# Kernel tuning notes

Hardware: AMD Instinct MI355X
Metric: run time of the kernel (lower is better)

The kernel has to match this reference:

```python
import jax, jax.numpy as jnp
import numpy as np

SENS = 200
DM = 128
NMAPS = 2
NLAYERS = 2
TH = 0.01
EPS = 1e-5
BATCH = 8
SEQ = 96
HEADS = 8


def setup_inputs() -> dict:
    key = jax.random.key(0)
    ks = jax.random.split(key, 8)
    x = jax.random.normal(ks[0], (BATCH, SENS, SEQ, DM), jnp.float32)
    attn_s = jax.random.uniform(ks[1], (1, BATCH, HEADS, SENS, SENS), jnp.float32)
    supports = jax.random.uniform(ks[2], (SENS, SENS), jnp.float32)
    W_conv = jax.random.normal(ks[3], (NMAPS, NLAYERS, DM, DM), jnp.float32) * 0.05
    b_conv = jnp.zeros((NMAPS, NLAYERS, DM), jnp.float32)
    bn_gamma = jnp.ones((NMAPS, DM), jnp.float32)
    bn_beta = jnp.zeros((NMAPS, DM), jnp.float32)
    W_out = jax.random.normal(ks[4], (NMAPS * DM, DM), jnp.float32) * 0.05
    b_out = jnp.zeros((DM,), jnp.float32)
    return dict(x=x, attn_s=attn_s, supports=supports, W_conv=W_conv,
                b_conv=b_conv, bn_gamma=bn_gamma, bn_beta=bn_beta,
                W_out=W_out, b_out=b_out)


def _process_map(A):
    # make_symmetric: lower triangle + mirrored strict lower triangle
    A = jnp.tril(A) + jnp.tril(A, -1).T
    # clamp: threshold on absolute value; note original returns |A| thresholded
    Aa = jnp.abs(A)
    A = jnp.where(Aa > TH, Aa, jnp.zeros_like(Aa))
    # SparseTensor.from_dense(A).t()
    return A.T


def _gcn_norm(adj_t):
    # GCNConv default: add self-loops (weight 1), symmetric D^-1/2 A D^-1/2
    A = adj_t + jnp.eye(adj_t.shape[0], dtype=adj_t.dtype)
    deg = A.sum(axis=1)
    d = jnp.where(deg > 0, jax.lax.rsqrt(deg), jnp.zeros_like(deg))
    return d[:, None] * A * d[None, :]


def reference(x, attn_s, supports, W_conv, b_conv, bn_gamma, bn_beta, W_out, b_out):
    B, N, S, D = x.shape
    # reshape_mat: [B,N,S,D] -> [B*S, N, D]
    xr = x.transpose(0, 2, 1, 3).reshape(B * S, N, D)

    # supports: [data map, adaptive map from attention (mean over batch, heads)]
    maps = [_process_map(supports), _process_map(attn_s[0].mean(axis=(0, 1)))]

    gcn_outputs = []
    for i in range(NMAPS):
        An = _gcn_norm(maps[i])  # [N,N]
        h = jnp.zeros_like(xr[..., :1]) * 0.0  # placeholder replaced below
        h = None
        for l in range(NLAYERS):
            xw = jnp.einsum('bnf,fg->bng', xr, W_conv[i, l])
            hl = jnp.einsum('mn,bng->bmg', An, xw) + b_conv[i, l]
            h = hl if h is None else h + hl
        # BatchNorm1d over feature channel (training-mode batch stats, biased var)
        mu = h.mean(axis=(0, 1))
        var = h.var(axis=(0, 1))
        hn = (h - mu) * jax.lax.rsqrt(var + EPS) * bn_gamma[i] + bn_beta[i]
        gcn_outputs.append(jax.nn.relu(hn))

    cat = jnp.concatenate(gcn_outputs, axis=-1)  # [B*S, N, NMAPS*DM]
    y = jax.nn.relu(jnp.einsum('bnc,cd->bnd', cat, W_out) + b_out)
    # inverse_reshape_mat: [B*S, N, D] -> [B, N, S, D]
    return y.reshape(B, S, N, D).transpose(0, 2, 1, 3)
```

## Files before the change

kernel.cpp:

```cpp
#include <hip/hip_runtime.h>

#define SENS 200
#define DM 128
#define SEQ 96
#define NB 8
#define BS 768
#define NTOT 153600
#define TH 0.01f
#define BN_EPS 1e-5f
#define MPAD 224
#define KP 208
#define XWROW 212
#define ASROW 76

typedef __attribute__((ext_vector_type(8)))  __bf16 bf16x8;
typedef __attribute__((ext_vector_type(4)))  __bf16 bf16x4;
typedef __attribute__((ext_vector_type(16))) float  f32x16;

__device__ __forceinline__ f32x16 mfma32(bf16x8 a, bf16x8 b, f32x16 c) {
    return __builtin_amdgcn_mfma_f32_32x32x16_bf16(a, b, c, 0, 0, 0);
}
__device__ __forceinline__ bf16x8 join8(bf16x4 a, bf16x4 b) {
    bf16x8 r;
    #pragma unroll
    for (int j = 0; j < 4; ++j) { r[j] = a[j]; r[j + 4] = b[j]; }
    return r;
}

__global__ void attn_mean_kernel(const float* __restrict__ attn, float* __restrict__ mapA) {
    int idx = blockIdx.x * 256 + threadIdx.x;
    if (idx >= SENS * SENS) return;
    float s = 0.f;
    #pragma unroll 8
    for (int q = 0; q < 64; ++q) s += attn[(size_t)q * SENS * SENS + idx];
    mapA[idx] = s * (1.0f / 64.0f);
}

__global__ void build_map_kernel(const float* __restrict__ supports, const float* __restrict__ mapA,
                                 float* __restrict__ M, float* __restrict__ deg) {
    __shared__ float red[256];
    int m = blockIdx.x, map = blockIdx.y, j = threadIdx.x;
    const float* src = (map == 0) ? supports : mapA;
    float v = 0.f;
    if (j < SENS) {
        float sym = (m >= j) ? src[m * SENS + j] : src[j * SENS + m];
        float a = fabsf(sym);
        v = (a > TH) ? a : 0.f;
        M[(size_t)map * SENS * SENS + m * SENS + j] = v;
    }
    red[j] = v;
    __syncthreads();
    for (int off = 128; off > 0; off >>= 1) {
        if (j < off) red[j] += red[j + off];
        __syncthreads();
    }
    if (j == 0) deg[map * SENS + m] = red[0] + 1.0f;
}

__global__ __launch_bounds__(256) void prep2_kernel(
    const float* __restrict__ x, const float* __restrict__ M, const float* __restrict__ deg,
    const float* __restrict__ W_conv, const float* __restrict__ b_conv,
    const float* __restrict__ W_out,
    __bf16* __restrict__ xk, __bf16* __restrict__ Anb,
    __bf16* __restrict__ Wt, __bf16* __restrict__ Wot,
    float* __restrict__ bsum, float* __restrict__ bnacc)
{
    const int bid = blockIdx.x, t = threadIdx.x;
    if (bid < BS) {
        const int bs = bid, b = bs / SEQ, s = bs % SEQ;
        const int fq = t & 31, sub = t >> 5;
        const float* xp = x + ((size_t)b * SENS) * SEQ * DM + (size_t)s * DM + fq * 4;
        __bf16* xo = xk + ((size_t)bs * 8 + (fq >> 2)) * MPAD * 16 + (fq & 3) * 4;
        for (int n = sub; n < MPAD; n += 8) {
            float4 v = make_float4(0.f, 0.f, 0.f, 0.f);
            if (n < SENS) v = *(const float4*)(xp + (size_t)n * SEQ * DM);
            bf16x4 o;
            o[0] = (__bf16)v.x; o[1] = (__bf16)v.y; o[2] = (__bf16)v.z; o[3] = (__bf16)v.w;
            *(bf16x4*)(xo + (size_t)n * 16) = o;
        }
    } else if (bid < BS + 2 * MPAD) {
        const int i = bid - BS, map = i / MPAD, m = i % MPAD;
        const int j = t;
        if (j < KP) {
            float val = 0.f;
            if (m < SENS && j < SENS) {
                float a = M[((size_t)map * SENS + m) * SENS + j] + ((m == j) ? 1.f : 0.f);
                val = rsqrtf(deg[map * SENS + m]) * a * rsqrtf(deg[map * SENS + j]);
            }
            Anb[(((size_t)map * 13 + (j >> 4)) * MPAD + m) * 16 + (j & 15)] = (__bf16)val;
        }
    } else {
        const int idx = (bid - (BS + 2 * MPAD)) * 256 + t;
        if (idx < 32768) {
            const int map = idx >> 14, g = (idx >> 7) & 127, f = idx & 127;
            const float* wp = W_conv + (size_t)map * 2 * DM * DM + f * DM + g;
            Wt[(((size_t)map * 8 + (f >> 4)) * DM + g) * 16 + (f & 15)] = (__bf16)(wp[0] + wp[DM * DM]);
        } else if (idx < 65536) {
            const int k = idx - 32768, d = k >> 8, c = k & 255;
            Wot[(((size_t)(c >> 4)) * DM + d) * 16 + (c & 15)] = (__bf16)W_out[c * DM + d];
        } else if (idx < 65792) {
            const int k = idx - 65536, map = k >> 7, g = k & 127;
            bsum[k] = b_conv[(map * 2) * DM + g] + b_conv[(map * 2 + 1) * DM + g];
        } else if (idx < 66304) {
            bnacc[idx - 65792] = 0.f;
        }
    }
}

__global__ __launch_bounds__(448) void conv_kernel(
    const __bf16* __restrict__ xk, const __bf16* __restrict__ Anb,
    const __bf16* __restrict__ Wt, const float* __restrict__ bsum,
    __bf16* __restrict__ h, float* __restrict__ bnacc)
{
    __shared__ __bf16 xw[128 * XWROW];
    const int bs = blockIdx.x, map = blockIdx.y;
    const int t = threadIdx.x, w = t >> 6, lane = t & 63;
    const int l31 = lane & 31, hi = lane >> 5;

    const __bf16* xb = xk + (((size_t)bs * 8) * MPAD + w * 32 + l31) * 16 + hi * 8;
    #pragma unroll
    for (int gh = 0; gh < 2; ++gh) {
        f32x16 acc[2];
        #pragma unroll
        for (int p = 0; p < 2; ++p)
            #pragma unroll
            for (int r = 0; r < 16; ++r) acc[p][r] = 0.f;
        const __bf16* wb = Wt + (((size_t)map * 8) * DM + gh * 64 + l31) * 16 + hi * 8;
        #pragma unroll
        for (int kc = 0; kc < 8; ++kc) {
            bf16x8 bfrag = *(const bf16x8*)(xb + (size_t)kc * MPAD * 16);
            #pragma unroll
            for (int p = 0; p < 2; ++p)
                acc[p] = mfma32(*(const bf16x8*)(wb + ((size_t)kc * DM + p * 32) * 16), bfrag, acc[p]);
        }
        if (w < 6 || l31 < 16) {
            #pragma unroll
            for (int p = 0; p < 2; ++p)
                #pragma unroll
                for (int r = 0; r < 16; ++r) {
                    const int row = gh * 64 + p * 32 + (r & 3) + 8 * (r >> 2) + 4 * hi;
                    xw[row * XWROW + w * 32 + l31] = (__bf16)acc[p][r];
                }
        }
    }
    __syncthreads();

    float bsn[4], bsq[4];
    const __bf16* ab = Anb + (((size_t)map * 13) * MPAD + w * 32 + l31) * 16 + hi * 8;
    #pragma unroll
    for (int cth = 0; cth < 2; ++cth) {
        f32x16 acc2[2];
        #pragma unroll
        for (int p = 0; p < 2; ++p)
            #pragma unroll
            for (int r = 0; r < 16; ++r) acc2[p][r] = 0.f;
        #pragma unroll
        for (int kc = 0; kc < 13; ++kc) {
            bf16x8 afrag = *(const bf16x8*)(ab + (size_t)kc * MPAD * 16);
            #pragma unroll
            for (int p = 0; p < 2; ++p) {
                const __bf16* pp = &xw[((cth * 2 + p) * 32 + l31) * XWROW + kc * 16 + hi * 8];
                acc2[p] = mfma32(afrag, join8(*(const bf16x4*)pp, *(const bf16x4*)(pp + 4)), acc2[p]);
            }
        }
        #pragma unroll
        for (int p = 0; p < 2; ++p) {
            const int ct = cth * 2 + p;
            const float bias = bsum[map * DM + ct * 32 + l31];
            bf16x8 h0, h1;
            float s = 0.f, q = 0.f;
            #pragma unroll
            for (int r = 0; r < 16; ++r) {
                const float v = acc2[p][r] + bias;
                if (r < 8) h0[r] = (__bf16)v; else h1[r - 8] = (__bf16)v;
                const int m = w * 32 + (r & 3) + 8 * (r >> 2) + 4 * hi;
                if (m < SENS) { s += v; q += v * v; }
            }
            __bf16* hp = h + ((((size_t)(bs * 2 + map) * 7 + w) * 4 + ct) * 64 + lane) * 16;
            *(bf16x8*)hp = h0;
            *(bf16x8*)(hp + 8) = h1;
            s += __shfl_xor(s, 32);
            q += __shfl_xor(q, 32);
            bsn[ct] = s; bsq[ct] = q;
        }
    }
    __syncthreads();
    float* red = (float*)xw;
    if (hi == 0) {
        #pragma unroll
        for (int ct = 0; ct < 4; ++ct) {
            red[(ct * 32 + l31) * 7 + w] = bsn[ct];
            red[(128 + ct * 32 + l31) * 7 + w] = bsq[ct];
        }
    }
    __syncthreads();
    if (t < 256) {
        const int sq = t >> 7, g = t & 127;
        float s = 0.f;
        #pragma unroll
        for (int k = 0; k < 7; ++k) s += red[(sq * 128 + g) * 7 + k];
        atomicAdd(&bnacc[sq * 256 + map * DM + g], s);
    }
}

__global__ __launch_bounds__(512) void out_kernel(
    const __bf16* __restrict__ h, const __bf16* __restrict__ Wot,
    const float* __restrict__ bnacc,
    const float* __restrict__ gamma, const float* __restrict__ beta,
    const float* __restrict__ b_out, float* __restrict__ out)
{
    __shared__ __bf16 As[MPAD * ASROW];
    __shared__ float sc_s[256], sh_s[256];
    const int bs = blockIdx.x;
    const int b = bs / SEQ, s = bs % SEQ;
    const int t = threadIdx.x, w = t >> 6, lane = t & 63;
    const int l31 = lane & 31, hi = lane >> 5;
    const int dct = w & 3, sbase = w >> 2;
    if (t < 256) {
        const float mu = bnacc[t] * (1.f / (float)NTOT);
        const float var = bnacc[256 + t] * (1.f / (float)NTOT) - mu * mu;
        const float sc = gamma[t] * rsqrtf(var + BN_EPS);
        sc_s[t] = sc;
        sh_s[t] = beta[t] - mu * sc;
    }

    f32x16 acc[4];
    {
        const float bo = b_out[dct * 32 + l31];
        #pragma unroll
        for (int i = 0; i < 4; ++i)
            #pragma unroll
            for (int r = 0; r < 16; ++r) acc[i][r] = bo;
    }
    for (int chunk = 0; chunk < 4; ++chunk) {
        const int map = chunk >> 1;
        __syncthreads();
        {
            const __bf16* hb = h + ((size_t)(bs * 2 + map) * 28 + (chunk & 1) * 2) * 1024;
            #pragma unroll
            for (int it = 0; it < 4; ++it) {
                const int idx = it * 512 + t;
                if (idx < 1792) {
                    const int half = idx & 1, lane_s = (idx >> 1) & 63;
                    const int ctl = (idx >> 7) & 1, strip = idx >> 8;
                    bf16x8 v = *(const bf16x8*)(hb + ((size_t)strip * 4 + ctl) * 1024 + lane_s * 16 + half * 8);
                    const int cl = ctl * 32 + (lane_s & 31);
                    const int cg = map * DM + (chunk & 1) * 64 + cl;
                    const float scv = sc_s[cg], shv = sh_s[cg];
                    const int mbase = strip * 32 + 4 * (lane_s >> 5) + 16 * half;
                    #pragma unroll
                    for (int q2 = 0; q2 < 8; ++q2) {
                        const int row = mbase + (q2 & 3) + 8 * (q2 >> 2);
                        const float fv = (float)v[q2] * scv + shv;
                        As[row * ASROW + cl] = (__bf16)fmaxf(fv, 0.f);
                    }
                }
            }
        }
        __syncthreads();
        #pragma unroll
        for (int kc = 0; kc < 4; ++kc) {
            bf16x8 bfrag = *(const bf16x8*)(Wot + (((size_t)(chunk * 4 + kc)) * DM + dct * 32 + l31) * 16 + hi * 8);
            #pragma unroll
            for (int i = 0; i < 4; ++i) {
                const int strip = sbase + 2 * i;
                if (strip >= 7) break;
                const __bf16* ap = &As[(strip * 32 + l31) * ASROW + kc * 16 + hi * 8];
                acc[i] = mfma32(join8(*(const bf16x4*)ap, *(const bf16x4*)(ap + 4)), bfrag, acc[i]);
            }
        }
    }
    #pragma unroll
    for (int i = 0; i < 4; ++i) {
        const int strip = sbase + 2 * i;
        if (strip >= 7) break;
        #pragma unroll
        for (int r = 0; r < 16; ++r) {
            const int m = strip * 32 + (r & 3) + 8 * (r >> 2) + 4 * hi;
            if (m < SENS)
                out[(((size_t)b * SENS + m) * SEQ + s) * DM + dct * 32 + l31] = fmaxf(acc[i][r], 0.f);
        }
    }
}

extern "C" void kernel_launch(void* const* d_in, const int* in_sizes, int n_in,
                              void* d_out, int out_size, void* d_ws, size_t ws_size,
                              hipStream_t stream) {
    const float* x        = (const float*)d_in[0];
    const float* attn     = (const float*)d_in[1];
    const float* supports = (const float*)d_in[2];
    const float* W_conv   = (const float*)d_in[3];
    const float* b_conv   = (const float*)d_in[4];
    const float* gamma    = (const float*)d_in[5];
    const float* beta     = (const float*)d_in[6];
    const float* W_out    = (const float*)d_in[7];
    const float* b_out    = (const float*)d_in[8];
    float* out = (float*)d_out;
    char* base = (char*)d_ws;

    float*  mapA  = (float*)(base + 0);
    float*  Mbuf  = (float*)(base + 160000);
    float*  deg   = (float*)(base + 480000);
    float*  bnacc = (float*)(base + 481664);
    float*  bsum  = (float*)(base + 483712);
    __bf16* Wt    = (__bf16*)(base + 484736);
    __bf16* Wot   = (__bf16*)(base + 550272);
    __bf16* Anb   = (__bf16*)(base + 615808);
    __bf16* xk    = (__bf16*)(base + 1048576);
    __bf16* h     = (__bf16*)(base + 45088768);

    attn_mean_kernel<<<157, 256, 0, stream>>>(attn, mapA);
    build_map_kernel<<<dim3(SENS, 2), 256, 0, stream>>>(supports, mapA, Mbuf, deg);
    prep2_kernel<<<BS + 2 * MPAD + 260, 256, 0, stream>>>(x, Mbuf, deg, W_conv, b_conv, W_out,
                                                          xk, Anb, Wt, Wot, bsum, bnacc);
    conv_kernel<<<dim3(BS, 2), 448, 0, stream>>>(xk, Anb, Wt, bsum, h, bnacc);
    out_kernel<<<BS, 512, 0, stream>>>(h, Wot, bnacc, gamma, beta, b_out, out);
}
```

Measured before the change: 282.9 us.

## Split conv blocks by map and feature half, separate coalesced x prep, double-buffer out stage

```diff
diff --git a/kernel.cpp b/kernel.cpp
--- a/kernel.cpp
+++ b/kernel.cpp
@@ -10,8 +10,7 @@
 #define BN_EPS 1e-5f
 #define MPAD 224
 #define KP 208
-#define XWROW 212
-#define ASROW 76
+#define ASROW 68
 
 typedef __attribute__((ext_vector_type(8)))  __bf16 bf16x8;
 typedef __attribute__((ext_vector_type(4)))  __bf16 bf16x4;
@@ -58,28 +57,15 @@
 }
 
 __global__ __launch_bounds__(256) void prep2_kernel(
-    const float* __restrict__ x, const float* __restrict__ M, const float* __restrict__ deg,
+    const float* __restrict__ M, const float* __restrict__ deg,
     const float* __restrict__ W_conv, const float* __restrict__ b_conv,
     const float* __restrict__ W_out,
-    __bf16* __restrict__ xk, __bf16* __restrict__ Anb,
-    __bf16* __restrict__ Wt, __bf16* __restrict__ Wot,
+    __bf16* __restrict__ Anb, __bf16* __restrict__ Wt, __bf16* __restrict__ Wot,
     float* __restrict__ bsum, float* __restrict__ bnacc)
 {
     const int bid = blockIdx.x, t = threadIdx.x;
-    if (bid < BS) {
-        const int bs = bid, b = bs / SEQ, s = bs % SEQ;
-        const int fq = t & 31, sub = t >> 5;
-        const float* xp = x + ((size_t)b * SENS) * SEQ * DM + (size_t)s * DM + fq * 4;
-        __bf16* xo = xk + ((size_t)bs * 8 + (fq >> 2)) * MPAD * 16 + (fq & 3) * 4;
-        for (int n = sub; n < MPAD; n += 8) {
-            float4 v = make_float4(0.f, 0.f, 0.f, 0.f);
-            if (n < SENS) v = *(const float4*)(xp + (size_t)n * SEQ * DM);
-            bf16x4 o;
-            o[0] = (__bf16)v.x; o[1] = (__bf16)v.y; o[2] = (__bf16)v.z; o[3] = (__bf16)v.w;
-            *(bf16x4*)(xo + (size_t)n * 16) = o;
-        }
-    } else if (bid < BS + 2 * MPAD) {
-        const int i = bid - BS, map = i / MPAD, m = i % MPAD;
+    if (bid < 2 * MPAD) {
+        const int map = bid / MPAD, m = bid % MPAD;
         const int j = t;
         if (j < KP) {
             float val = 0.f;
@@ -90,7 +76,7 @@
             Anb[(((size_t)map * 13 + (j >> 4)) * MPAD + m) * 16 + (j & 15)] = (__bf16)val;
         }
     } else {
-        const int idx = (bid - (BS + 2 * MPAD)) * 256 + t;
+        const int idx = (bid - 2 * MPAD) * 256 + t;
         if (idx < 32768) {
             const int map = idx >> 14, g = (idx >> 7) & 127, f = idx & 127;
             const float* wp = W_conv + (size_t)map * 2 * DM * DM + f * DM + g;
@@ -107,99 +93,155 @@
     }
 }
 
-__global__ __launch_bounds__(448) void conv_kernel(
+__global__ __launch_bounds__(256) void xprep_kernel(const float* __restrict__ x,
+                                                    __bf16* __restrict__ xk) {
+    const int n = blockIdx.x, b = blockIdx.y, t = threadIdx.x;
+    const float* xp = x + ((size_t)b * SENS + n) * SEQ * DM;
+    #pragma unroll 4
+    for (int it = 0; it < 12; ++it) {
+        const int idx = it * 1024 + t * 4;
+        const int s = idx >> 7, f = idx & 127;
+        float4 v = make_float4(0.f, 0.f, 0.f, 0.f);
+        if (n < SENS) v = *(const float4*)(xp + idx);
+        bf16x4 o;
+        o[0] = (__bf16)v.x; o[1] = (__bf16)v.y; o[2] = (__bf16)v.z; o[3] = (__bf16)v.w;
+        *(bf16x4*)(xk + (((size_t)(b * SEQ + s) * 8 + (f >> 4)) * MPAD + n) * 16 + (f & 15)) = o;
+    }
+}
+
+__global__ __launch_bounds__(448, 6) void conv_kernel(
     const __bf16* __restrict__ xk, const __bf16* __restrict__ Anb,
     const __bf16* __restrict__ Wt, const float* __restrict__ bsum,
     __bf16* __restrict__ h, float* __restrict__ bnacc)
 {
-    __shared__ __bf16 xw[128 * XWROW];
-    const int bs = blockIdx.x, map = blockIdx.y;
+    __shared__ __bf16 xw[64 * KP];
+    const int bx = blockIdx.x;
+    const int bs = bx >> 2, map = (bx >> 1) & 1, gh = bx & 1;
     const int t = threadIdx.x, w = t >> 6, lane = t & 63;
     const int l31 = lane & 31, hi = lane >> 5;
 
-    const __bf16* xb = xk + (((size_t)bs * 8) * MPAD + w * 32 + l31) * 16 + hi * 8;
-    #pragma unroll
-    for (int gh = 0; gh < 2; ++gh) {
+    {
         f32x16 acc[2];
         #pragma unroll
         for (int p = 0; p < 2; ++p)
             #pragma unroll
             for (int r = 0; r < 16; ++r) acc[p][r] = 0.f;
+        const __bf16* xb = xk + (((size_t)bs * 8) * MPAD + w * 32 + l31) * 16 + hi * 8;
         const __bf16* wb = Wt + (((size_t)map * 8) * DM + gh * 64 + l31) * 16 + hi * 8;
         #pragma unroll
-        for (int kc = 0; kc < 8; ++kc) {
-            bf16x8 bfrag = *(const bf16x8*)(xb + (size_t)kc * MPAD * 16);
-            #pragma unroll
-            for (int p = 0; p < 2; ++p)
-                acc[p] = mfma32(*(const bf16x8*)(wb + ((size_t)kc * DM + p * 32) * 16), bfrag, acc[p]);
-        }
-        if (w < 6 || l31 < 16) {
+        for (int kh = 0; kh < 2; ++kh) {
+            bf16x8 bfr[4];
+            #pragma unroll
+            for (int q = 0; q < 4; ++q)
+                bfr[q] = *(const bf16x8*)(xb + (size_t)(kh * 4 + q) * MPAD * 16);
+            #pragma unroll
+            for (int q = 0; q < 4; ++q) {
+                const __bf16* wp = wb + (size_t)(kh * 4 + q) * DM * 16;
+                acc[0] = mfma32(*(const bf16x8*)wp, bfr[q], acc[0]);
+                acc[1] = mfma32(*(const bf16x8*)(wp + 32 * 16), bfr[q], acc[1]);
+            }
+        }
+        const int n = w * 32 + l31;
+        if (n < KP) {
             #pragma unroll
             for (int p = 0; p < 2; ++p)
                 #pragma unroll
                 for (int r = 0; r < 16; ++r) {
-                    const int row = gh * 64 + p * 32 + (r & 3) + 8 * (r >> 2) + 4 * hi;
-                    xw[row * XWROW + w * 32 + l31] = (__bf16)acc[p][r];
+                    const int g = p * 32 + (r & 3) + 8 * (r >> 2) + 4 * hi;
+                    xw[g * KP + n] = (__bf16)acc[p][r];
                 }
         }
     }
     __syncthreads();
 
-    float bsn[4], bsq[4];
-    const __bf16* ab = Anb + (((size_t)map * 13) * MPAD + w * 32 + l31) * 16 + hi * 8;
-    #pragma unroll
-    for (int cth = 0; cth < 2; ++cth) {
-        f32x16 acc2[2];
-        #pragma unroll
-        for (int p = 0; p < 2; ++p)
-            #pragma unroll
-            for (int r = 0; r < 16; ++r) acc2[p][r] = 0.f;
+    f32x16 acc2[2];
+    #pragma unroll
+    for (int p = 0; p < 2; ++p)
+        #pragma unroll
+        for (int r = 0; r < 16; ++r) acc2[p][r] = 0.f;
+    {
+        const __bf16* ab = Anb + (((size_t)map * 13) * MPAD + w * 32 + l31) * 16 + hi * 8;
         #pragma unroll
         for (int kc = 0; kc < 13; ++kc) {
             bf16x8 afrag = *(const bf16x8*)(ab + (size_t)kc * MPAD * 16);
             #pragma unroll
             for (int p = 0; p < 2; ++p) {
-                const __bf16* pp = &xw[((cth * 2 + p) * 32 + l31) * XWROW + kc * 16 + hi * 8];
-                acc2[p] = mfma32(afrag, join8(*(const bf16x4*)pp, *(const bf16x4*)(pp + 4)), acc2[p]);
-            }
-        }
-        #pragma unroll
-        for (int p = 0; p < 2; ++p) {
-            const int ct = cth * 2 + p;
-            const float bias = bsum[map * DM + ct * 32 + l31];
-            bf16x8 h0, h1;
-            float s = 0.f, q = 0.f;
-            #pragma unroll
-            for (int r = 0; r < 16; ++r) {
-                const float v = acc2[p][r] + bias;
-                if (r < 8) h0[r] = (__bf16)v; else h1[r - 8] = (__bf16)v;
-                const int m = w * 32 + (r & 3) + 8 * (r >> 2) + 4 * hi;
-                if (m < SENS) { s += v; q += v * v; }
-            }
-            __bf16* hp = h + ((((size_t)(bs * 2 + map) * 7 + w) * 4 + ct) * 64 + lane) * 16;
-            *(bf16x8*)hp = h0;
-            *(bf16x8*)(hp + 8) = h1;
-            s += __shfl_xor(s, 32);
-            q += __shfl_xor(q, 32);
-            bsn[ct] = s; bsq[ct] = q;
-        }
+                bf16x8 bfrag = *(const bf16x8*)(xw + (p * 32 + l31) * KP + kc * 16 + hi * 8);
+                acc2[p] = mfma32(afrag, bfrag, acc2[p]);
+            }
+        }
+    }
+    float bsn[2], bsq[2];
+    #pragma unroll
+    for (int p = 0; p < 2; ++p) {
+        const float bias = bsum[map * DM + gh * 64 + p * 32 + l31];
+        bf16x8 h0, h1;
+        float s = 0.f, q = 0.f;
+        #pragma unroll
+        for (int r = 0; r < 16; ++r) {
+            const float v = acc2[p][r] + bias;
+            if (r < 8) h0[r] = (__bf16)v; else h1[r - 8] = (__bf16)v;
+            const int m = w * 32 + (r & 3) + 8 * (r >> 2) + 4 * hi;
+            if (m < SENS) { s += v; q += v * v; }
+        }
+        __bf16* hp = h + ((((size_t)(bs * 2 + map) * 7 + w) * 4 + (gh * 2 + p)) * 64 + lane) * 16;
+        *(bf16x8*)hp = h0;
+        *(bf16x8*)(hp + 8) = h1;
+        s += __shfl_xor(s, 32);
+        q += __shfl_xor(q, 32);
+        bsn[p] = s; bsq[p] = q;
     }
     __syncthreads();
     float* red = (float*)xw;
     if (hi == 0) {
         #pragma unroll
-        for (int ct = 0; ct < 4; ++ct) {
-            red[(ct * 32 + l31) * 7 + w] = bsn[ct];
-            red[(128 + ct * 32 + l31) * 7 + w] = bsq[ct];
-        }
-    }
-    __syncthreads();
-    if (t < 256) {
-        const int sq = t >> 7, g = t & 127;
+        for (int p = 0; p < 2; ++p) {
+            red[(p * 32 + l31) * 7 + w] = bsn[p];
+            red[(64 + p * 32 + l31) * 7 + w] = bsq[p];
+        }
+    }
+    __syncthreads();
+    if (t < 128) {
+        const int sq = t >> 6, g = t & 63;
         float s = 0.f;
         #pragma unroll
-        for (int k = 0; k < 7; ++k) s += red[(sq * 128 + g) * 7 + k];
-        atomicAdd(&bnacc[sq * 256 + map * DM + g], s);
+        for (int k = 0; k < 7; ++k) s += red[(sq * 64 + g) * 7 + k];
+        atomicAdd(&bnacc[sq * 256 + map * DM + gh * 64 + g], s);
+    }
+}
+
+__device__ __forceinline__ void out_stage(int cn, int t, int bs,
+                                          const __bf16* __restrict__ h,
+                                          const float* sc_s, const float* sh_s,
+                                          __bf16* dst)
+{
+    const int mapn = cn >> 1;
+    const __bf16* hb = h + ((size_t)(bs * 2 + mapn) * 28 + (cn & 1) * 2) * 1024;
+    bf16x8 vv[4];
+    #pragma unroll
+    for (int it = 0; it < 4; ++it) {
+        const int idx = it * 512 + t;
+        if (idx < 1792)
+            vv[it] = *(const bf16x8*)(hb + ((size_t)(idx >> 8) * 4 + ((idx >> 7) & 1)) * 1024
+                                          + ((idx >> 1) & 63) * 16 + (idx & 1) * 8);
+    }
+    #pragma unroll
+    for (int it = 0; it < 4; ++it) {
+        const int idx = it * 512 + t;
+        if (idx < 1792) {
+            const int half = idx & 1, lane_s = (idx >> 1) & 63;
+            const int ctl = (idx >> 7) & 1, strip = idx >> 8;
+            const int cl = ctl * 32 + (lane_s & 31);
+            const int cg = mapn * DM + (cn & 1) * 64 + cl;
+            const float scv = sc_s[cg], shv = sh_s[cg];
+            const int mbase = strip * 32 + 4 * (lane_s >> 5) + 16 * half;
+            #pragma unroll
+            for (int q2 = 0; q2 < 8; ++q2) {
+                const int row = mbase + (q2 & 3) + 8 * (q2 >> 2);
+                const float fv = (float)vv[it][q2] * scv + shv;
+                dst[row * ASROW + cl] = (__bf16)fmaxf(fv, 0.f);
+            }
+        }
     }
 }
 
@@ -209,7 +251,7 @@
     const float* __restrict__ gamma, const float* __restrict__ beta,
     const float* __restrict__ b_out, float* __restrict__ out)
 {
-    __shared__ __bf16 As[MPAD * ASROW];
+    __shared__ __bf16 As[2][MPAD * ASROW];
     __shared__ float sc_s[256], sh_s[256];
     const int bs = blockIdx.x;
     const int b = bs / SEQ, s = bs % SEQ;
@@ -223,7 +265,6 @@
         sc_s[t] = sc;
         sh_s[t] = beta[t] - mu * sc;
     }
-
     f32x16 acc[4];
     {
         const float bo = b_out[dct * 32 + l31];
@@ -232,43 +273,23 @@
             #pragma unroll
             for (int r = 0; r < 16; ++r) acc[i][r] = bo;
     }
-    for (int chunk = 0; chunk < 4; ++chunk) {
-        const int map = chunk >> 1;
-        __syncthreads();
-        {
-            const __bf16* hb = h + ((size_t)(bs * 2 + map) * 28 + (chunk & 1) * 2) * 1024;
-            #pragma unroll
-            for (int it = 0; it < 4; ++it) {
-                const int idx = it * 512 + t;
-                if (idx < 1792) {
-                    const int half = idx & 1, lane_s = (idx >> 1) & 63;
-                    const int ctl = (idx >> 7) & 1, strip = idx >> 8;
-                    bf16x8 v = *(const bf16x8*)(hb + ((size_t)strip * 4 + ctl) * 1024 + lane_s * 16 + half * 8);
-                    const int cl = ctl * 32 + (lane_s & 31);
-                    const int cg = map * DM + (chunk & 1) * 64 + cl;
-                    const float scv = sc_s[cg], shv = sh_s[cg];
-                    const int mbase = strip * 32 + 4 * (lane_s >> 5) + 16 * half;
-                    #pragma unroll
-                    for (int q2 = 0; q2 < 8; ++q2) {
-                        const int row = mbase + (q2 & 3) + 8 * (q2 >> 2);
-                        const float fv = (float)v[q2] * scv + shv;
-                        As[row * ASROW + cl] = (__bf16)fmaxf(fv, 0.f);
-                    }
-                }
-            }
-        }
-        __syncthreads();
+    __syncthreads();
+    out_stage(0, t, bs, h, sc_s, sh_s, &As[0][0]);
+    __syncthreads();
+    for (int c = 0; c < 4; ++c) {
         #pragma unroll
         for (int kc = 0; kc < 4; ++kc) {
-            bf16x8 bfrag = *(const bf16x8*)(Wot + (((size_t)(chunk * 4 + kc)) * DM + dct * 32 + l31) * 16 + hi * 8);
+            bf16x8 bfrag = *(const bf16x8*)(Wot + ((size_t)(c * 4 + kc) * DM + dct * 32 + l31) * 16 + hi * 8);
             #pragma unroll
             for (int i = 0; i < 4; ++i) {
                 const int strip = sbase + 2 * i;
                 if (strip >= 7) break;
-                const __bf16* ap = &As[(strip * 32 + l31) * ASROW + kc * 16 + hi * 8];
+                const __bf16* ap = &As[c & 1][(strip * 32 + l31) * ASROW + kc * 16 + hi * 8];
                 acc[i] = mfma32(join8(*(const bf16x4*)ap, *(const bf16x4*)(ap + 4)), bfrag, acc[i]);
             }
         }
+        if (c < 3) out_stage(c + 1, t, bs, h, sc_s, sh_s, &As[(c + 1) & 1][0]);
+        __syncthreads();
     }
     #pragma unroll
     for (int i = 0; i < 4; ++i) {
@@ -311,8 +332,9 @@
 
     attn_mean_kernel<<<157, 256, 0, stream>>>(attn, mapA);
     build_map_kernel<<<dim3(SENS, 2), 256, 0, stream>>>(supports, mapA, Mbuf, deg);
-    prep2_kernel<<<BS + 2 * MPAD + 260, 256, 0, stream>>>(x, Mbuf, deg, W_conv, b_conv, W_out,
-                                                          xk, Anb, Wt, Wot, bsum, bnacc);
-    conv_kernel<<<dim3(BS, 2), 448, 0, stream>>>(xk, Anb, Wt, bsum, h, bnacc);
+    prep2_kernel<<<2 * MPAD + 260, 256, 0, stream>>>(Mbuf, deg, W_conv, b_conv, W_out,
+                                                     Anb, Wt, Wot, bsum, bnacc);
+    xprep_kernel<<<dim3(MPAD, NB), 256, 0, stream>>>(x, xk);
+    conv_kernel<<<BS * 4, 448, 0, stream>>>(xk, Anb, Wt, bsum, h, bnacc);
     out_kernel<<<BS, 512, 0, stream>>>(h, Wot, bnacc, gamma, beta, b_out, out);
 }
```

Result: slower. 289.6 us (+2.4%).
